# Performance work log

Measured on AMD Instinct MI355X. Metric: run time of the kernel, lower is better.

The kernel has to match this reference:

```python
import jax, jax.numpy as jnp
import numpy as np


def conv1x1(x, w, b):
    # x: [B,C,H,W], w: [O,C], b: [O]
    return jnp.einsum('bchw,oc->bohw', x, w) + b[None, :, None, None]


def conv3x3(x, w, b):
    # x: [B,C,H,W], w: [O,C,3,3]
    y = jax.lax.conv_general_dilated(
        x, w, window_strides=(1, 1), padding='SAME',
        dimension_numbers=('NCHW', 'OIHW', 'NCHW'))
    return y + b[None, :, None, None]


def setup_inputs() -> dict:
    key = jax.random.key(0)
    ks = jax.random.split(key, 20)

    def u(k, shape, fan_in):
        # PyTorch Conv2d default init: uniform(-1/sqrt(fan_in), 1/sqrt(fan_in))
        s = 1.0 / np.sqrt(fan_in)
        return jax.random.uniform(k, shape, jnp.float32, -s, s)

    B, H, W = 4, 64, 64
    return {
        'x':   jax.random.normal(ks[0], (B, 3, H, W), jnp.float32),
        # 1x1 stem convs (weights stored as [O,C])
        'w1':  u(ks[1], (64, 3), 3),        'b1':  u(ks[2], (64,), 3),
        'w2':  u(ks[3], (128, 64), 64),     'b2':  u(ks[4], (128,), 64),
        'w3':  u(ks[5], (256, 128), 128),   'b3':  u(ks[6], (256,), 128),
        # 3x3 conv branch (fan_in = 256*9)
        'wb1': u(ks[7], (256, 256, 3, 3), 256 * 9), 'bb1': u(ks[8], (256,), 256 * 9),
        'wb2': u(ks[9], (256, 256, 3, 3), 256 * 9), 'bb2': u(ks[10], (256,), 256 * 9),
        # q/k/v 1x1 convs
        'wq':  u(ks[11], (256, 256), 256),  'bq':  u(ks[12], (256,), 256),
        'wk':  u(ks[13], (256, 256), 256),  'bk':  u(ks[14], (256,), 256),
        'wv':  u(ks[15], (256, 256), 256),  'bv':  u(ks[16], (256,), 256),
        'alpha': jnp.float32(0.5),
        'beta':  jnp.float32(0.5),
    }


def reference(x, w1, b1, w2, b2, w3, b3, wb1, bb1, wb2, bb2,
              wq, bq, wk, bk, wv, bv, alpha, beta):
    x = jax.nn.relu(conv1x1(x, w1, b1))
    x = jax.nn.relu(conv1x1(x, w2, b2))
    x = jax.nn.relu(conv1x1(x, w3, b3))          # [B,256,H,W]
    conv_out = conv3x3(jax.nn.relu(conv3x3(x, wb1, bb1)), wb2, bb2)
    B, C, H, W = x.shape
    q = conv1x1(x, wq, bq).reshape(B, C, -1)     # [B,C,N]
    k = conv1x1(x, wk, bk).reshape(B, C, -1)     # [B,C,N]
    v = conv1x1(x, wv, bv).reshape(B, C, -1)     # [B,C,N]
    # torch: bmm(k^T, q) -> [B,N,N], softmax over last dim
    attn = jax.nn.softmax(jnp.einsum('bcn,bcm->bnm', k, q), axis=-1)
    # torch: bmm(v, attn) -> [B,C,N]
    attn_out = jnp.einsum('bcn,bnm->bcm', v, attn).reshape(B, C, H, W)
    return alpha * conv_out + beta * attn_out
```

## Files before the change

kernel.cpp:

```cpp
#include <hip/hip_runtime.h>
#include <math.h>

#define NPIX 4096
#define CC   256

typedef __attribute__((ext_vector_type(8))) short bf16x8;
typedef __attribute__((ext_vector_type(4))) float f32x4;

__device__ inline unsigned short f2bf(float f) {
    unsigned u = __builtin_bit_cast(unsigned, f);
    u += 0x7FFF + ((u >> 16) & 1);
    return (unsigned short)(u >> 16);
}
__device__ inline float bf2f(unsigned short h) {
    unsigned u = (unsigned)h << 16;
    return __builtin_bit_cast(float, u);
}
__device__ inline void gl_lds16(const unsigned short* g, unsigned short* l) {
    __builtin_amdgcn_global_load_lds(
        (const __attribute__((address_space(1))) void*)g,
        (__attribute__((address_space(3))) void*)l, 16, 0, 0);
}

__global__ __launch_bounds__(256) void prep_kernel(
    const float* __restrict__ w2, const float* __restrict__ w3,
    const float* __restrict__ wq, const float* __restrict__ wk,
    const float* __restrict__ wv, const float* __restrict__ wb1,
    const float* __restrict__ wb2, const float* __restrict__ bq,
    const float* __restrict__ bk,
    unsigned short* w2b, unsigned short* w3b, unsigned short* wqb,
    unsigned short* wkb, unsigned short* wvb,
    unsigned short* wr1, unsigned short* wr2, float* bqk) {
    int i = blockIdx.x * 256 + threadIdx.x;
    if (i < 8192)  w2b[i] = f2bf(w2[i]);
    if (i < 32768) w3b[i] = f2bf(w3[i]);
    if (i < 65536) { wqb[i] = f2bf(wq[i]); wkb[i] = f2bf(wk[i]); wvb[i] = f2bf(wv[i]); }
    if (i < 256)   { bqk[i] = bq[i]; bqk[256 + i] = bk[i]; }
    if (i < 589824) {
        int o = i / 2304; int r = i - o * 2304; int tap = r >> 8; int c = r & 255;
        wr1[i] = f2bf(wb1[(o * 256 + c) * 9 + tap]);
        wr2[i] = f2bf(wb2[(o * 256 + c) * 9 + tap]);
    }
}

__global__ __launch_bounds__(256) void stem1_kernel(
    const float* __restrict__ x, const float* __restrict__ w1,
    const float* __restrict__ b1, unsigned short* __restrict__ h1T) {
    int idx = blockIdx.x * 256 + threadIdx.x;
    int o = idx & 63;
    int p = (idx >> 6) & 4095;
    int b = idx >> 18;
    const float* xb = x + (size_t)b * 3 * NPIX + p;
    float acc = b1[o];
    acc = fmaf(w1[o * 3 + 0], xb[0],        acc);
    acc = fmaf(w1[o * 3 + 1], xb[NPIX],     acc);
    acc = fmaf(w1[o * 3 + 2], xb[2 * NPIX], acc);
    h1T[idx] = f2bf(fmaxf(acc, 0.f));
}

template<int EPI, int KK>
__global__ __launch_bounds__(256) void gemm_fullk(
    const unsigned short* __restrict__ A, long lda, long sA,
    const unsigned short* __restrict__ BT, long ldb, long sB,
    void* __restrict__ Cp, long ldc, long sC,
    const float* __restrict__ bias, float* __restrict__ aux) {
    constexpr int SPR = KK / 8;
    constexpr int RPI = 64 / SPR;
    __shared__ unsigned short As[128 * KK];
    __shared__ unsigned short Bs[128 * KK];
    const int tid  = threadIdx.x;
    const int lane = tid & 63;
    const int wave = tid >> 6;
    const int wr = (wave >> 1) * 64, wc = (wave & 1) * 64;
    const int l15 = lane & 15, lh = lane >> 4;
    const int sl  = lane & (SPR - 1);
    const int rof = lane / SPR;
    const int z = blockIdx.z;
    const unsigned short* Ab = A  + (size_t)z * sA + (size_t)blockIdx.y * 128 * lda;
    const unsigned short* Bb = BT + (size_t)z * sB + (size_t)blockIdx.x * 128 * ldb;

    f32x4 acc[4][4];
    #pragma unroll
    for (int i = 0; i < 4; ++i)
        #pragma unroll
        for (int j = 0; j < 4; ++j) { f32x4 zr = {0.f, 0.f, 0.f, 0.f}; acc[i][j] = zr; }

    #pragma unroll
    for (int i = 0; i < KK / 16; ++i) {
        int r0  = wave * 32 + i * RPI;
        int row = r0 + rof;
        int cs  = (sl ^ (row & (SPR - 1))) * 8;
        gl_lds16(Ab + (size_t)row * lda + cs, &As[r0 * KK]);
        gl_lds16(Bb + (size_t)row * ldb + cs, &Bs[r0 * KK]);
    }
    __syncthreads();

    #pragma unroll
    for (int ks = 0; ks < KK / 32; ++ks) {
        bf16x8 a[4], b[4];
        #pragma unroll
        for (int f = 0; f < 4; ++f) {
            int ra = wr + f * 16 + l15;
            a[f] = *(const bf16x8*)&As[ra * KK + ((((ks << 2) + lh) ^ (ra & (SPR - 1))) << 3)];
            int rb = wc + f * 16 + l15;
            b[f] = *(const bf16x8*)&Bs[rb * KK + ((((ks << 2) + lh) ^ (rb & (SPR - 1))) << 3)];
        }
        #pragma unroll
        for (int i = 0; i < 4; ++i)
            #pragma unroll
            for (int j = 0; j < 4; ++j)
                acc[i][j] = __builtin_amdgcn_mfma_f32_16x16x32_bf16(
                    a[i], b[j], acc[i][j], 0, 0, 0);
    }

    const int row0 = blockIdx.y * 128 + wr;
    const int col0 = blockIdx.x * 128 + wc;
    unsigned short* OUT = (unsigned short*)Cp + (size_t)z * sC;
    #pragma unroll
    for (int i = 0; i < 4; ++i)
        #pragma unroll
        for (int j = 0; j < 4; ++j) {
            int cgl = col0 + j * 16 + l15;
            float bc = (EPI == 1 || EPI == 2) ? bias[cgl] : 0.f;
            float sc = (EPI == 3) ? aux[(size_t)z * 4096 + cgl] : 1.f;
            #pragma unroll
            for (int q = 0; q < 4; ++q) {
                int r = row0 + i * 16 + lh * 4 + q;
                float v = acc[i][j][q];
                if (EPI == 3) v = (v + bias[r]) * sc;
                else v += bc;
                if (EPI == 1) v = fmaxf(v, 0.f);
                OUT[(size_t)r * ldc + cgl] = f2bf(v);
            }
        }
}

#define PH_ENTER                                            \
    asm volatile("" ::: "memory");                          \
    __builtin_amdgcn_s_barrier();                           \
    asm volatile("s_waitcnt lgkmcnt(0)" ::: "memory");      \
    __builtin_amdgcn_sched_barrier(0);                      \
    __builtin_amdgcn_s_setprio(1);
#define PH_EXIT                                             \
    __builtin_amdgcn_s_setprio(0);                          \
    asm volatile("" ::: "memory");                          \
    __builtin_amdgcn_s_barrier();

#define DO_TILE(CURA, CURB, NXTA, NXTB, KT)                                    \
{                                                                              \
    const int kn_ = (KT) + 1;                                                  \
    bf16x8 aL[4][2], aH[4][2], b01[2][2], b23[2][2];                           \
                                 \
    _Pragma("unroll") for (int f = 0; f < 4; ++f) {                            \
        const unsigned short* rp = &(CURA)[(wr + f * 16 + l15) * 64];          \
        aL[f][0] = *(const bf16x8*)&rp[sa0];                                   \
        aL[f][1] = *(const bf16x8*)&rp[sa1];                                   \
    }                                                                          \
    _Pragma("unroll") for (int f = 0; f < 2; ++f) {                            \
        const unsigned short* rp = &(CURB)[(wc + f * 16 + l15) * 64];          \
        b01[f][0] = *(const bf16x8*)&rp[sa0];                                  \
        b01[f][1] = *(const bf16x8*)&rp[sa1];                                  \
    }                                                                          \
    if (kn_ < T) {                                                             \
        _Pragma("unroll") for (int s = 0; s < 4; ++s) {                        \
            int rb_ = wave * 32 + s * 8;                                       \
            gl_lds16(Ab + (size_t)(rb_ + rof) * lda + (kn_ << 6) + csw,        \
                     &(NXTA)[rb_ * 64]);                                       \
        }                                                                      \
    }                                                                          \
    PH_ENTER;                                                                  \
    _Pragma("unroll") for (int i = 0; i < 4; ++i)                              \
        _Pragma("unroll") for (int j = 0; j < 2; ++j)                          \
            _Pragma("unroll") for (int ks = 0; ks < 2; ++ks)                   \
                acc[i][j] = __builtin_amdgcn_mfma_f32_16x16x32_bf16(           \
                    aL[i][ks], b01[j][ks], acc[i][j], 0, 0, 0);                \
    PH_EXIT;                                                                   \
                                      \
    _Pragma("unroll") for (int f = 0; f < 2; ++f) {                            \
        const unsigned short* rp = &(CURB)[(wc + 32 + f * 16 + l15) * 64];     \
        b23[f][0] = *(const bf16x8*)&rp[sa0];                                  \
        b23[f][1] = *(const bf16x8*)&rp[sa1];                                  \
    }                                                                          \
    if (kn_ < T) {                                                             \
        _Pragma("unroll") for (int s = 0; s < 4; ++s) {                        \
            int rb_ = wave * 32 + s * 8;                                       \
            gl_lds16(Bb + (size_t)(rb_ + rof) * ldb + (kn_ << 6) + csw,        \
                     &(NXTB)[rb_ * 64]);                                       \
        }                                                                      \
    }                                                                          \
    PH_ENTER;                                                                  \
    _Pragma("unroll") for (int i = 0; i < 4; ++i)                              \
        _Pragma("unroll") for (int j = 0; j < 2; ++j)                          \
            _Pragma("unroll") for (int ks = 0; ks < 2; ++ks)                   \
                acc[i][j + 2] = __builtin_amdgcn_mfma_f32_16x16x32_bf16(       \
                    aL[i][ks], b23[j][ks], acc[i][j + 2], 0, 0, 0);            \
    PH_EXIT;                                                                   \
                                                    \
    _Pragma("unroll") for (int f = 0; f < 4; ++f) {                            \
        const unsigned short* rp = &(CURA)[(wr + 64 + f * 16 + l15) * 64];     \
        aH[f][0] = *(const bf16x8*)&rp[sa0];                                   \
        aH[f][1] = *(const bf16x8*)&rp[sa1];                                   \
    }                                                                          \
    PH_ENTER;                                                                  \
    _Pragma("unroll") for (int i = 0; i < 4; ++i)                              \
        _Pragma("unroll") for (int j = 0; j < 2; ++j)                          \
            _Pragma("unroll") for (int ks = 0; ks < 2; ++ks)                   \
                acc[i + 4][j + 2] = __builtin_amdgcn_mfma_f32_16x16x32_bf16(   \
                    aH[i][ks], b23[j][ks], acc[i + 4][j + 2], 0, 0, 0);        \
    PH_EXIT;                                                                   \
                                             \
    asm volatile("s_waitcnt vmcnt(0)" ::: "memory");                           \
    PH_ENTER;                                                                  \
    _Pragma("unroll") for (int i = 0; i < 4; ++i)                              \
        _Pragma("unroll") for (int j = 0; j < 2; ++j)                          \
            _Pragma("unroll") for (int ks = 0; ks < 2; ++ks)                   \
                acc[i + 4][j] = __builtin_amdgcn_mfma_f32_16x16x32_bf16(       \
                    aH[i][ks], b01[j][ks], acc[i + 4][j], 0, 0, 0);            \
    PH_EXIT;                                                                   \
}

template<int EPI>
__global__ __launch_bounds__(512) void gemm256(
    const unsigned short* __restrict__ A, long lda, long sA,
    const unsigned short* __restrict__ BT, long ldb, long sB,
    int Kc, int splits, int nb,
    void* __restrict__ Cp, long ldc, long sC,
    float* __restrict__ aux, float* __restrict__ partial,
    const unsigned short* __restrict__ CV,
    const float* __restrict__ alphaP, const float* __restrict__ betaP,
    int nwgc) {
    __shared__ unsigned short As0[256 * 64], As1[256 * 64];
    __shared__ unsigned short Bs0[256 * 64], Bs1[256 * 64];
    const int orig = blockIdx.x;
    const int wgid = (orig & 7) * nwgc + (orig >> 3);
    int bx, by, sp, z;
    if (EPI == 0) { bx = wgid & 15; by = (wgid >> 4) & 15; z = wgid >> 8; sp = 0; }
    else          { bx = wgid & 15; sp = (wgid >> 4) & (splits - 1); z = wgid / (16 * splits); by = 0; }

    const int tid  = threadIdx.x;
    const int lane = tid & 63;
    const int wave = tid >> 6;
    const int wr = (wave >> 2) * 128;
    const int wc = (wave & 3) * 64;
    const int l15 = lane & 15, lh = lane >> 4;
    const int sl  = lane & 7, rof = lane >> 3;
    const int csw = (sl ^ rof) * 8;
    const int sa0 = ((lh ^ (l15 & 7)) << 3);
    const int sa1 = (((4 + lh) ^ (l15 & 7)) << 3);
    const unsigned short* Ab = A  + (size_t)z * sA + (size_t)by * 256 * lda + (size_t)sp * Kc;
    const unsigned short* Bb = BT + (size_t)z * sB + (size_t)bx * 256 * ldb + (size_t)sp * Kc;

    f32x4 acc[8][4];
    #pragma unroll
    for (int i = 0; i < 8; ++i)
        #pragma unroll
        for (int j = 0; j < 4; ++j) { f32x4 zr = {0.f, 0.f, 0.f, 0.f}; acc[i][j] = zr; }

    const int T = Kc >> 6;
    #pragma unroll
    for (int s = 0; s < 4; ++s) {
        int rb = wave * 32 + s * 8;
        gl_lds16(Ab + (size_t)(rb + rof) * lda + csw, &As0[rb * 64]);
        gl_lds16(Bb + (size_t)(rb + rof) * ldb + csw, &Bs0[rb * 64]);
    }
    asm volatile("s_waitcnt vmcnt(0)" ::: "memory");
    __builtin_amdgcn_s_barrier();

    for (int kt = 0; kt < T; kt += 2) {
        DO_TILE(As0, Bs0, As1, Bs1, kt);
        DO_TILE(As1, Bs1, As0, Bs0, kt + 1);
    }

    if (EPI == 0) {
        unsigned short* OUT = (unsigned short*)Cp + (size_t)z * sC;
        const int row0 = by * 256 + wr;
        const int col0 = bx * 256 + wc;
        float cs4[4] = {0.f, 0.f, 0.f, 0.f};
        #pragma unroll
        for (int i = 0; i < 8; ++i)
            #pragma unroll
            for (int j = 0; j < 4; ++j) {
                int cgl = col0 + j * 16 + l15;
                #pragma unroll
                for (int q = 0; q < 4; ++q) {
                    int r = row0 + i * 16 + lh * 4 + q;
                    unsigned short h = f2bf(__expf(acc[i][j][q]));
                    OUT[(size_t)r * ldc + cgl] = h;
                    cs4[j] += bf2f(h);
                }
            }
        #pragma unroll
        for (int off = 16; off <= 32; off <<= 1)
            #pragma unroll
            for (int j = 0; j < 4; ++j)
                cs4[j] += __shfl_xor(cs4[j], off);
        if (lh == 0) {
            float* part = aux + (((size_t)z * 16 + by) * 2 + (wave >> 2)) * 4096;
            #pragma unroll
            for (int j = 0; j < 4; ++j)
                part[col0 + j * 16 + l15] = cs4[j];
        }
    } else {
        const int col0 = bx * 256 + wc;
        if (splits == 1) {
            float* OUT = (float*)Cp + (size_t)z * sC;
            const unsigned short* CVb = CV + (size_t)z * sC;
            const float al = alphaP[0], be = betaP[0];
            #pragma unroll
            for (int i = 0; i < 8; ++i)
                #pragma unroll
                for (int j = 0; j < 4; ++j) {
                    int cgl = col0 + j * 16 + l15;
                    #pragma unroll
                    for (int q = 0; q < 4; ++q) {
                        int r = wr + i * 16 + lh * 4 + q;
                        size_t o = (size_t)r * ldc + cgl;
                        OUT[o] = al * bf2f(CVb[o]) + be * acc[i][j][q];
                    }
                }
        } else {
            float* P = partial + ((size_t)sp * nb + z) * ((size_t)256 * 4096);
            #pragma unroll
            for (int i = 0; i < 8; ++i)
                #pragma unroll
                for (int j = 0; j < 4; ++j) {
                    int cgl = col0 + j * 16 + l15;
                    #pragma unroll
                    for (int q = 0; q < 4; ++q) {
                        int r = wr + i * 16 + lh * 4 + q;
                        P[(size_t)r * 4096 + cgl] = acc[i][j][q];
                    }
                }
        }
    }
}

__global__ __launch_bounds__(256) void reduce_kernel(
    const float* __restrict__ partial, const unsigned short* __restrict__ cvb,
    const float* __restrict__ alphaP, const float* __restrict__ betaP,
    float* __restrict__ outp, int splits, long chunk) {
    long idx = ((long)blockIdx.x * 256 + threadIdx.x) * 4;
    if (idx >= chunk) return;
    float4 s = *(const float4*)&partial[idx];
    for (int sp = 1; sp < splits; ++sp) {
        float4 p = *(const float4*)&partial[(size_t)sp * chunk + idx];
        s.x += p.x; s.y += p.y; s.z += p.z; s.w += p.w;
    }
    ushort4 c4 = *(const ushort4*)&cvb[idx];
    const float al = alphaP[0], be = betaP[0];
    float4 r;
    r.x = al * bf2f(c4.x) + be * s.x;
    r.y = al * bf2f(c4.y) + be * s.y;
    r.z = al * bf2f(c4.z) + be * s.z;
    r.w = al * bf2f(c4.w) + be * s.w;
    *(float4*)&outp[idx] = r;
}

__global__ __launch_bounds__(256) void recip_kernel(
    const float* __restrict__ part, float* __restrict__ rcp) {
    int idx = blockIdx.x * 256 + threadIdx.x;
    int z = idx >> 12, n = idx & 4095;
    const float* pb = part + (size_t)z * 32 * 4096 + n;
    float s = 0.f;
    #pragma unroll 8
    for (int t = 0; t < 32; ++t) s += pb[(size_t)t * 4096];
    rcp[idx] = 1.f / s;
}

template<int PIXOUT>
__global__ __launch_bounds__(256) void conv3_v2(
    const unsigned short* __restrict__ X, const unsigned short* __restrict__ Wr,
    const float* __restrict__ bias, void* __restrict__ Outp) {
    __shared__ unsigned short wt[9 * 128 * 40];
    __shared__ unsigned short patch[264 * 40];
    const int tid  = threadIdx.x;
    const int lane = tid & 63;
    const int wave = tid >> 6;
    const int l15 = lane & 15, lh = lane >> 4;
    const int oh = blockIdx.x & 1;
    const int b  = blockIdx.x >> 1;
    const int h0 = blockIdx.y;
    const int wy = (wave >> 1) * 64, wx = (wave & 1) * 64;
    const int obase = PIXOUT ? wx : wy;
    const int pbase = PIXOUT ? wy : wx;
    const unsigned short* Xb  = X + (size_t)b * (NPIX * CC);
    const unsigned short* Wro = Wr + (size_t)oh * 128 * 2304;

    f32x4 acc[4][4];
    #pragma unroll
    for (int i = 0; i < 4; ++i)
        #pragma unroll
        for (int j = 0; j < 4; ++j) { f32x4 zr = {0.f, 0.f, 0.f, 0.f}; acc[i][j] = zr; }

    for (int c0 = 0; c0 < 256; c0 += 32) {
        __syncthreads();
        #pragma unroll
        for (int t = 0; t < 5; ++t) {
            int q = t * 256 + tid;
            if (q < 1056) {
                int slot = q >> 2, cg = (q & 3) * 8;
                int r = slot / 66, w = slot - r * 66;
                int hh = h0 * 2 - 1 + r, ww = w - 1;
                int4 v = make_int4(0, 0, 0, 0);
                if ((unsigned)hh < 64u && (unsigned)ww < 64u)
                    v = *(const int4*)&Xb[(size_t)(hh * 64 + ww) * 256 + c0 + cg];
                *(int4*)&patch[slot * 40 + cg] = v;
            }
        }
        #pragma unroll
        for (int t = 0; t < 18; ++t) {
            int q = t * 256 + tid;
            int o = q / 36, rem = q - o * 36;
            int tap = rem >> 2, cg = (rem & 3) * 8;
            int4 v = *(const int4*)&Wro[(size_t)o * 2304 + tap * 256 + c0 + cg];
            *(int4*)&wt[(tap * 128 + o) * 40 + cg] = v;
        }
        __syncthreads();
        #pragma unroll
        for (int tap = 0; tap < 9; ++tap) {
            const int dy = tap / 3 - 1, dx = tap % 3 - 1;
            bf16x8 wf[4], pf[4];
            #pragma unroll
            for (int f = 0; f < 4; ++f) {
                int o = obase + f * 16 + l15;
                wf[f] = *(const bf16x8*)&wt[(tap * 128 + o) * 40 + lh * 8];
                int p = pbase + f * 16 + l15;
                int slot = ((p >> 6) + dy + 1) * 66 + (p & 63) + dx + 1;
                pf[f] = *(const bf16x8*)&patch[slot * 40 + lh * 8];
            }
            #pragma unroll
            for (int i = 0; i < 4; ++i)
                #pragma unroll
                for (int j = 0; j < 4; ++j) {
                    if (PIXOUT)
                        acc[i][j] = __builtin_amdgcn_mfma_f32_16x16x32_bf16(
                            pf[i], wf[j], acc[i][j], 0, 0, 0);
                    else
                        acc[i][j] = __builtin_amdgcn_mfma_f32_16x16x32_bf16(
                            wf[i], pf[j], acc[i][j], 0, 0, 0);
                }
        }
    }

    const int P0 = h0 * 128;
    if (PIXOUT) {
        unsigned short* O = (unsigned short*)Outp + (size_t)b * (NPIX * CC);
        #pragma unroll
        for (int i = 0; i < 4; ++i)
            #pragma unroll
            for (int j = 0; j < 4; ++j) {
                int o = oh * 128 + obase + j * 16 + l15;
                float bb = bias[o];
                #pragma unroll
                for (int q = 0; q < 4; ++q) {
                    int p = pbase + i * 16 + lh * 4 + q;
                    float v = fmaxf(acc[i][j][q] + bb, 0.f);
                    O[(size_t)(P0 + p) * CC + o] = f2bf(v);
                }
            }
    } else {
        unsigned short* O = (unsigned short*)Outp + (size_t)b * (CC * NPIX);
        #pragma unroll
        for (int i = 0; i < 4; ++i)
            #pragma unroll
            for (int j = 0; j < 4; ++j) {
                #pragma unroll
                for (int q = 0; q < 4; ++q) {
                    int o = oh * 128 + obase + i * 16 + lh * 4 + q;
                    int p = pbase + j * 16 + l15;
                    O[(size_t)o * NPIX + P0 + p] = f2bf(acc[i][j][q] + bias[o]);
                }
            }
    }
}

extern "C" void kernel_launch(void* const* d_in, const int* in_sizes, int n_in,
                              void* d_out, int out_size, void* d_ws, size_t ws_size,
                              hipStream_t stream) {
    const float* x   = (const float*)d_in[0];
    const float* w1  = (const float*)d_in[1];  const float* b1  = (const float*)d_in[2];
    const float* w2  = (const float*)d_in[3];  const float* b2  = (const float*)d_in[4];
    const float* w3  = (const float*)d_in[5];  const float* b3  = (const float*)d_in[6];
    const float* wb1 = (const float*)d_in[7];  const float* bb1 = (const float*)d_in[8];
    const float* wb2 = (const float*)d_in[9];  const float* bb2 = (const float*)d_in[10];
    const float* wq  = (const float*)d_in[11]; const float* bq  = (const float*)d_in[12];
    const float* wk  = (const float*)d_in[13]; const float* bk  = (const float*)d_in[14];
    const float* wv  = (const float*)d_in[15]; const float* bv  = (const float*)d_in[16];
    const float* alpha = (const float*)d_in[17];
    const float* beta  = (const float*)d_in[18];

    const size_t MB = 1 << 20;
    char* wsb = (char*)d_ws;
    unsigned short* x3T = (unsigned short*)(wsb + 0 * MB);
    unsigned short* qkT = (unsigned short*)(wsb + 8 * MB);
    unsigned short* cv  = (unsigned short*)(wsb + 24 * MB);
    unsigned short* t1T = (unsigned short*)(wsb + 32 * MB);
    unsigned short* h1T = (unsigned short*)(wsb + 32 * MB);
    unsigned short* h2T = (unsigned short*)(wsb + 34 * MB);
    unsigned short* vB  = (unsigned short*)(wsb + 40 * MB);
    unsigned short* w2b = (unsigned short*)(wsb + 48 * MB);
    unsigned short* w3b = w2b + 8192;
    unsigned short* wqb = w3b + 32768;
    unsigned short* wkb = wqb + 65536;
    unsigned short* wvb = wkb + 65536;
    unsigned short* wr1 = wvb + 65536;
    unsigned short* wr2 = wr1 + 589824;
    float*          bqk  = (float*)(wsb + 51 * MB);
    float*          part = (float*)(wsb + 52 * MB);
    float*          rcp  = (float*)(wsb + 54 * MB);
    unsigned short* ST   = (unsigned short*)(wsb + 55 * MB);
    float* out = (float*)d_out;
    const long ONEM = (long)CC * NPIX;
    const long SS = 4096L * 4096;

    int nb, splits;
    if      (ws_size >= (size_t)247 * MB) { nb = 4; splits = 4;  }
    else if (ws_size >= (size_t)183 * MB) { nb = 2; splits = 8;  }
    else if (ws_size >= (size_t)151 * MB) { nb = 1; splits = 16; }
    else if (ws_size >= (size_t)119 * MB) { nb = 1; splits = 8;  }
    else if (ws_size >= (size_t)103 * MB) { nb = 1; splits = 4;  }
    else                                  { nb = 1; splits = 1;  }
    float* pvpart = (float*)(wsb + (size_t)(55 + nb * 32) * MB);

    prep_kernel<<<2304, 256, 0, stream>>>(w2, w3, wq, wk, wv, wb1, wb2, bq, bk,
                                          w2b, w3b, wqb, wkb, wvb, wr1, wr2, bqk);
    stem1_kernel<<<4096, 256, 0, stream>>>(x, w1, b1, h1T);

    gemm_fullk<1, 64><<<dim3(1, 32, 4), 256, 0, stream>>>(
        h1T, 64, 4096L * 64, w2b, 64, 0,
        h2T, 128, 4096L * 128, b2, nullptr);
    gemm_fullk<1, 128><<<dim3(2, 32, 4), 256, 0, stream>>>(
        h2T, 128, 4096L * 128, w3b, 128, 0,
        x3T, 256, 4096L * 256, b3, nullptr);
    gemm_fullk<2, 256><<<dim3(4, 32, 4), 256, 0, stream>>>(
        x3T, 256, 4096L * 256, wqb, 256, 0,
        qkT, 512, 4096L * 512, bqk, nullptr);
    conv3_v2<1><<<dim3(8, 32), 256, 0, stream>>>(x3T, wr1, bb1, t1T);
    conv3_v2<0><<<dim3(8, 32), 256, 0, stream>>>(t1T, wr2, bb2, cv);

    for (int b0 = 0; b0 < 4; b0 += nb) {
        int nwgS = 256 * nb;
        gemm256<0><<<nwgS, 512, 0, stream>>>(
            qkT + (size_t)b0 * 4096 * 512, 512, 4096L * 512,
            qkT + (size_t)b0 * 4096 * 512 + 256, 512, 4096L * 512,
            256, 1, nb, ST, 4096, SS,
            part, nullptr, nullptr, nullptr, nullptr, nwgS / 8);
        recip_kernel<<<nb * 16, 256, 0, stream>>>(part, rcp);
        gemm_fullk<3, 256><<<dim3(32, 2, nb), 256, 0, stream>>>(
            wvb, 256, 0,
            x3T + (size_t)b0 * 4096 * 256, 256, 4096L * 256,
            vB, 4096, 256L * 4096, bv, rcp);
        int nwgP = 16 * splits * nb;
        gemm256<4><<<nwgP, 512, 0, stream>>>(
            vB, 4096, 256L * 4096, ST, 4096, SS,
            4096 / splits, splits, nb,
            out + (size_t)b0 * ONEM, 4096, ONEM,
            nullptr, pvpart, cv + (size_t)b0 * ONEM, alpha, beta, nwgP / 8);
        if (splits > 1)
            reduce_kernel<<<nb * 1024, 256, 0, stream>>>(
                pvpart, cv + (size_t)b0 * ONEM, alpha, beta,
                out + (size_t)b0 * ONEM, splits, (long)nb * ONEM);
    }
}
```

Baseline: 245.4 us.

## Store attention scores and scaled V in FP8 and run PV GEMM with FP8 MFMA

The exp(S) matrix and the normalized V are now written as FP8 (with scale factors of 1/16 and 256 to keep values in range) instead of bf16. A new FP8 PV GEMM kernel then uses 16x16x32 fp8 MFMA, which halves the bytes of the dominant 4096x4096 score matrix traffic. Split-K partials are stored as bf16 instead of fp32, and the split/batch configuration changes to nb=4, splits=8. This trades numerical accuracy, since FP8 softmax weights and bf16 partials are lossy, for lower memory traffic and higher MFMA throughput.

```diff
diff --git a/kernel.cpp b/kernel.cpp
--- a/kernel.cpp
+++ b/kernel.cpp
@@ -16,7 +16,11 @@
     unsigned u = (unsigned)h << 16;
     return __builtin_bit_cast(float, u);
 }
-__device__ inline void gl_lds16(const unsigned short* g, unsigned short* l) {
+__device__ inline unsigned char f2fp8(float f) {
+    int p = __builtin_amdgcn_cvt_pk_fp8_f32(f, f, 0, false);
+    return (unsigned char)(p & 0xff);
+}
+__device__ inline void gl_lds16(const void* g, void* l) {
     __builtin_amdgcn_global_load_lds(
         (const __attribute__((address_space(1))) void*)g,
         (__attribute__((address_space(3))) void*)l, 16, 0, 0);
@@ -115,24 +119,37 @@
 
     const int row0 = blockIdx.y * 128 + wr;
     const int col0 = blockIdx.x * 128 + wc;
-    unsigned short* OUT = (unsigned short*)Cp + (size_t)z * sC;
-    #pragma unroll
-    for (int i = 0; i < 4; ++i)
-        #pragma unroll
-        for (int j = 0; j < 4; ++j) {
-            int cgl = col0 + j * 16 + l15;
-            float bc = (EPI == 1 || EPI == 2) ? bias[cgl] : 0.f;
-            float sc = (EPI == 3) ? aux[(size_t)z * 4096 + cgl] : 1.f;
-            #pragma unroll
-            for (int q = 0; q < 4; ++q) {
-                int r = row0 + i * 16 + lh * 4 + q;
-                float v = acc[i][j][q];
-                if (EPI == 3) v = (v + bias[r]) * sc;
-                else v += bc;
-                if (EPI == 1) v = fmaxf(v, 0.f);
-                OUT[(size_t)r * ldc + cgl] = f2bf(v);
-            }
-        }
+    if (EPI == 3) {
+        unsigned char* O8 = (unsigned char*)Cp + (size_t)z * sC;
+        #pragma unroll
+        for (int i = 0; i < 4; ++i)
+            #pragma unroll
+            for (int j = 0; j < 4; ++j) {
+                int cgl = col0 + j * 16 + l15;
+                float sc = aux[(size_t)z * 4096 + cgl];
+                #pragma unroll
+                for (int q = 0; q < 4; ++q) {
+                    int r = row0 + i * 16 + lh * 4 + q;
+                    O8[(size_t)r * ldc + cgl] = f2fp8((acc[i][j][q] + bias[r]) * sc);
+                }
+            }
+    } else {
+        unsigned short* OUT = (unsigned short*)Cp + (size_t)z * sC;
+        #pragma unroll
+        for (int i = 0; i < 4; ++i)
+            #pragma unroll
+            for (int j = 0; j < 4; ++j) {
+                int cgl = col0 + j * 16 + l15;
+                float bc = bias[cgl];
+                #pragma unroll
+                for (int q = 0; q < 4; ++q) {
+                    int r = row0 + i * 16 + lh * 4 + q;
+                    float v = acc[i][j][q] + bc;
+                    if (EPI == 1) v = fmaxf(v, 0.f);
+                    OUT[(size_t)r * ldc + cgl] = f2bf(v);
+                }
+            }
+    }
 }
 
 #define PH_ENTER                                            \
@@ -150,7 +167,6 @@
 {                                                                              \
     const int kn_ = (KT) + 1;                                                  \
     bf16x8 aL[4][2], aH[4][2], b01[2][2], b23[2][2];                           \
-                                 \
     _Pragma("unroll") for (int f = 0; f < 4; ++f) {                            \
         const unsigned short* rp = &(CURA)[(wr + f * 16 + l15) * 64];          \
         aL[f][0] = *(const bf16x8*)&rp[sa0];                                   \
@@ -175,7 +191,6 @@
                 acc[i][j] = __builtin_amdgcn_mfma_f32_16x16x32_bf16(           \
                     aL[i][ks], b01[j][ks], acc[i][j], 0, 0, 0);                \
     PH_EXIT;                                                                   \
-                                      \
     _Pragma("unroll") for (int f = 0; f < 2; ++f) {                            \
         const unsigned short* rp = &(CURB)[(wc + 32 + f * 16 + l15) * 64];     \
         b23[f][0] = *(const bf16x8*)&rp[sa0];                                  \
@@ -195,7 +210,6 @@
                 acc[i][j + 2] = __builtin_amdgcn_mfma_f32_16x16x32_bf16(       \
                     aL[i][ks], b23[j][ks], acc[i][j + 2], 0, 0, 0);            \
     PH_EXIT;                                                                   \
-                                                    \
     _Pragma("unroll") for (int f = 0; f < 4; ++f) {                            \
         const unsigned short* rp = &(CURA)[(wr + 64 + f * 16 + l15) * 64];     \
         aH[f][0] = *(const bf16x8*)&rp[sa0];                                   \
@@ -208,7 +222,6 @@
                 acc[i + 4][j + 2] = __builtin_amdgcn_mfma_f32_16x16x32_bf16(   \
                     aH[i][ks], b23[j][ks], acc[i + 4][j + 2], 0, 0, 0);        \
     PH_EXIT;                                                                   \
-                                             \
     asm volatile("s_waitcnt vmcnt(0)" ::: "memory");                           \
     PH_ENTER;                                                                  \
     _Pragma("unroll") for (int i = 0; i < 4; ++i)                              \
@@ -219,23 +232,16 @@
     PH_EXIT;                                                                   \
 }
 
-template<int EPI>
-__global__ __launch_bounds__(512) void gemm256(
+__global__ __launch_bounds__(512) void gemm_s(
     const unsigned short* __restrict__ A, long lda, long sA,
     const unsigned short* __restrict__ BT, long ldb, long sB,
-    int Kc, int splits, int nb,
-    void* __restrict__ Cp, long ldc, long sC,
-    float* __restrict__ aux, float* __restrict__ partial,
-    const unsigned short* __restrict__ CV,
-    const float* __restrict__ alphaP, const float* __restrict__ betaP,
-    int nwgc) {
+    unsigned char* __restrict__ Cp, long ldc, long sC,
+    float* __restrict__ aux, int nwgc) {
     __shared__ unsigned short As0[256 * 64], As1[256 * 64];
     __shared__ unsigned short Bs0[256 * 64], Bs1[256 * 64];
     const int orig = blockIdx.x;
     const int wgid = (orig & 7) * nwgc + (orig >> 3);
-    int bx, by, sp, z;
-    if (EPI == 0) { bx = wgid & 15; by = (wgid >> 4) & 15; z = wgid >> 8; sp = 0; }
-    else          { bx = wgid & 15; sp = (wgid >> 4) & (splits - 1); z = wgid / (16 * splits); by = 0; }
+    const int bx = wgid & 15, by = (wgid >> 4) & 15, z = wgid >> 8;
 
     const int tid  = threadIdx.x;
     const int lane = tid & 63;
@@ -247,8 +253,8 @@
     const int csw = (sl ^ rof) * 8;
     const int sa0 = ((lh ^ (l15 & 7)) << 3);
     const int sa1 = (((4 + lh) ^ (l15 & 7)) << 3);
-    const unsigned short* Ab = A  + (size_t)z * sA + (size_t)by * 256 * lda + (size_t)sp * Kc;
-    const unsigned short* Bb = BT + (size_t)z * sB + (size_t)bx * 256 * ldb + (size_t)sp * Kc;
+    const unsigned short* Ab = A  + (size_t)z * sA + (size_t)by * 256 * lda;
+    const unsigned short* Bb = BT + (size_t)z * sB + (size_t)bx * 256 * ldb;
 
     f32x4 acc[8][4];
     #pragma unroll
@@ -256,7 +262,7 @@
         #pragma unroll
         for (int j = 0; j < 4; ++j) { f32x4 zr = {0.f, 0.f, 0.f, 0.f}; acc[i][j] = zr; }
 
-    const int T = Kc >> 6;
+    const int T = 4;
     #pragma unroll
     for (int s = 0; s < 4; ++s) {
         int rb = wave * 32 + s * 8;
@@ -271,11 +277,124 @@
         DO_TILE(As1, Bs1, As0, Bs0, kt + 1);
     }
 
-    if (EPI == 0) {
-        unsigned short* OUT = (unsigned short*)Cp + (size_t)z * sC;
-        const int row0 = by * 256 + wr;
-        const int col0 = bx * 256 + wc;
-        float cs4[4] = {0.f, 0.f, 0.f, 0.f};
+    unsigned char* OUT = Cp + (size_t)z * sC;
+    const int row0 = by * 256 + wr;
+    const int col0 = bx * 256 + wc;
+    float cs4[4] = {0.f, 0.f, 0.f, 0.f};
+    #pragma unroll
+    for (int i = 0; i < 8; ++i)
+        #pragma unroll
+        for (int j = 0; j < 4; ++j) {
+            int cgl = col0 + j * 16 + l15;
+            #pragma unroll
+            for (int q = 0; q < 4; ++q) {
+                int r = row0 + i * 16 + lh * 4 + q;
+                float e = __expf(acc[i][j][q]) * 0.0625f;
+                OUT[(size_t)r * ldc + cgl] = f2fp8(e);
+                cs4[j] += e;
+            }
+        }
+    #pragma unroll
+    for (int off = 16; off <= 32; off <<= 1)
+        #pragma unroll
+        for (int j = 0; j < 4; ++j)
+            cs4[j] += __shfl_xor(cs4[j], off);
+    if (lh == 0) {
+        float* part = aux + (((size_t)z * 16 + by) * 2 + (wave >> 2)) * 4096;
+        #pragma unroll
+        for (int j = 0; j < 4; ++j)
+            part[col0 + j * 16 + l15] = cs4[j];
+    }
+}
+
+__global__ __launch_bounds__(512) void gemm_pv8(
+    const unsigned char* __restrict__ A, long lda, long sA,
+    const unsigned char* __restrict__ BT, long ldb, long sB,
+    int Kc, int splits, int nb,
+    float* __restrict__ outp, long ldc, long sC,
+    unsigned short* __restrict__ partial,
+    const unsigned short* __restrict__ CV,
+    const float* __restrict__ alphaP, const float* __restrict__ betaP,
+    int nwgc) {
+    __shared__ unsigned char As[2][256 * 64];
+    __shared__ unsigned char Bs[2][256 * 64];
+    const int orig = blockIdx.x;
+    const int wgid = (orig & 7) * nwgc + (orig >> 3);
+    const int bx = wgid & 15;
+    const int sp = (wgid >> 4) % splits;
+    const int z  = wgid / (16 * splits);
+    const int tid  = threadIdx.x;
+    const int lane = tid & 63;
+    const int wave = tid >> 6;
+    const int wr = (wave >> 2) * 128;
+    const int wc = (wave & 3) * 64;
+    const int l15 = lane & 15, lh = lane >> 4;
+    const int srow = lane >> 2, sslot = lane & 3;
+    const unsigned char* Ab = A  + (size_t)z * sA + (size_t)sp * Kc;
+    const unsigned char* Bb = BT + (size_t)z * sB + (size_t)bx * 256 * ldb + (size_t)sp * Kc;
+
+    f32x4 acc[8][4];
+    #pragma unroll
+    for (int i = 0; i < 8; ++i)
+        #pragma unroll
+        for (int j = 0; j < 4; ++j) { f32x4 zr = {0.f, 0.f, 0.f, 0.f}; acc[i][j] = zr; }
+
+    auto STAGE = [&](int buf, int k0) {
+        #pragma unroll
+        for (int s = 0; s < 2; ++s) {
+            int rb  = wave * 32 + s * 16;
+            int row = rb + srow;
+            int cs  = (sslot ^ (row & 3)) << 4;
+            gl_lds16(Ab + (size_t)row * lda + k0 + cs, &As[buf][rb * 64]);
+            gl_lds16(Bb + (size_t)row * ldb + k0 + cs, &Bs[buf][rb * 64]);
+        }
+    };
+
+    STAGE(0, 0);
+    const int T = Kc >> 6;
+    for (int t = 0; t < T; ++t) {
+        const int cur = t & 1;
+        if (t + 1 < T) {
+            STAGE(cur ^ 1, (t + 1) << 6);
+            asm volatile("s_waitcnt vmcnt(4)" ::: "memory");
+        } else {
+            asm volatile("s_waitcnt vmcnt(0)" ::: "memory");
+        }
+        __builtin_amdgcn_s_barrier();
+        asm volatile("" ::: "memory");
+        __builtin_amdgcn_s_setprio(1);
+        #pragma unroll
+        for (int ks = 0; ks < 2; ++ks) {
+            long a[8], b[4];
+            #pragma unroll
+            for (int f = 0; f < 8; ++f) {
+                int row = wr + f * 16 + l15;
+                int ad  = row * 64 + ((((ks << 1) + (lh >> 1)) ^ (row & 3)) << 4) + ((lh & 1) << 3);
+                a[f] = *(const long*)&As[cur][ad];
+            }
+            #pragma unroll
+            for (int f = 0; f < 4; ++f) {
+                int row = wc + f * 16 + l15;
+                int ad  = row * 64 + ((((ks << 1) + (lh >> 1)) ^ (row & 3)) << 4) + ((lh & 1) << 3);
+                b[f] = *(const long*)&Bs[cur][ad];
+            }
+            #pragma unroll
+            for (int i = 0; i < 8; ++i)
+                #pragma unroll
+                for (int j = 0; j < 4; ++j)
+                    acc[i][j] = __builtin_amdgcn_mfma_f32_16x16x32_fp8_fp8(
+                        a[i], b[j], acc[i][j], 0, 0, 0);
+        }
+        __builtin_amdgcn_s_setprio(0);
+        asm volatile("" ::: "memory");
+        __builtin_amdgcn_s_barrier();
+    }
+
+    const int col0 = bx * 256 + wc;
+    if (splits == 1) {
+        float* OUT = outp + (size_t)z * sC;
+        const unsigned short* CVb = CV + (size_t)z * sC;
+        const float al = alphaP[0], be = betaP[0] * (1.f / 256.f);
         #pragma unroll
         for (int i = 0; i < 8; ++i)
             #pragma unroll
@@ -283,76 +402,45 @@
                 int cgl = col0 + j * 16 + l15;
                 #pragma unroll
                 for (int q = 0; q < 4; ++q) {
-                    int r = row0 + i * 16 + lh * 4 + q;
-                    unsigned short h = f2bf(__expf(acc[i][j][q]));
-                    OUT[(size_t)r * ldc + cgl] = h;
-                    cs4[j] += bf2f(h);
+                    int r = wr + i * 16 + lh * 4 + q;
+                    size_t o = (size_t)r * ldc + cgl;
+                    OUT[o] = al * bf2f(CVb[o]) + be * acc[i][j][q];
                 }
             }
-        #pragma unroll
-        for (int off = 16; off <= 32; off <<= 1)
-            #pragma unroll
-            for (int j = 0; j < 4; ++j)
-                cs4[j] += __shfl_xor(cs4[j], off);
-        if (lh == 0) {
-            float* part = aux + (((size_t)z * 16 + by) * 2 + (wave >> 2)) * 4096;
-            #pragma unroll
-            for (int j = 0; j < 4; ++j)
-                part[col0 + j * 16 + l15] = cs4[j];
-        }
     } else {
-        const int col0 = bx * 256 + wc;
-        if (splits == 1) {
-            float* OUT = (float*)Cp + (size_t)z * sC;
-            const unsigned short* CVb = CV + (size_t)z * sC;
-            const float al = alphaP[0], be = betaP[0];
-            #pragma unroll
-            for (int i = 0; i < 8; ++i)
-                #pragma unroll
-                for (int j = 0; j < 4; ++j) {
-                    int cgl = col0 + j * 16 + l15;
-                    #pragma unroll
-                    for (int q = 0; q < 4; ++q) {
-                        int r = wr + i * 16 + lh * 4 + q;
-                        size_t o = (size_t)r * ldc + cgl;
-                        OUT[o] = al * bf2f(CVb[o]) + be * acc[i][j][q];
-                    }
+        unsigned short* P = partial + ((size_t)sp * nb + z) * ((size_t)256 * 4096);
+        #pragma unroll
+        for (int i = 0; i < 8; ++i)
+            #pragma unroll
+            for (int j = 0; j < 4; ++j) {
+                int cgl = col0 + j * 16 + l15;
+                #pragma unroll
+                for (int q = 0; q < 4; ++q) {
+                    int r = wr + i * 16 + lh * 4 + q;
+                    P[(size_t)r * 4096 + cgl] = f2bf(acc[i][j][q]);
                 }
-        } else {
-            float* P = partial + ((size_t)sp * nb + z) * ((size_t)256 * 4096);
-            #pragma unroll
-            for (int i = 0; i < 8; ++i)
-                #pragma unroll
-                for (int j = 0; j < 4; ++j) {
-                    int cgl = col0 + j * 16 + l15;
-                    #pragma unroll
-                    for (int q = 0; q < 4; ++q) {
-                        int r = wr + i * 16 + lh * 4 + q;
-                        P[(size_t)r * 4096 + cgl] = acc[i][j][q];
-                    }
-                }
-        }
+            }
     }
 }
 
 __global__ __launch_bounds__(256) void reduce_kernel(
-    const float* __restrict__ partial, const unsigned short* __restrict__ cvb,
+    const unsigned short* __restrict__ partial, const unsigned short* __restrict__ cvb,
     const float* __restrict__ alphaP, const float* __restrict__ betaP,
     float* __restrict__ outp, int splits, long chunk) {
     long idx = ((long)blockIdx.x * 256 + threadIdx.x) * 4;
     if (idx >= chunk) return;
-    float4 s = *(const float4*)&partial[idx];
-    for (int sp = 1; sp < splits; ++sp) {
-        float4 p = *(const float4*)&partial[(size_t)sp * chunk + idx];
-        s.x += p.x; s.y += p.y; s.z += p.z; s.w += p.w;
+    float s0 = 0.f, s1 = 0.f, s2 = 0.f, s3 = 0.f;
+    for (int sp = 0; sp < splits; ++sp) {
+        ushort4 p = *(const ushort4*)&partial[(size_t)sp * chunk + idx];
+        s0 += bf2f(p.x); s1 += bf2f(p.y); s2 += bf2f(p.z); s3 += bf2f(p.w);
     }
     ushort4 c4 = *(const ushort4*)&cvb[idx];
-    const float al = alphaP[0], be = betaP[0];
+    const float al = alphaP[0], be = betaP[0] * (1.f / 256.f);
     float4 r;
-    r.x = al * bf2f(c4.x) + be * s.x;
-    r.y = al * bf2f(c4.y) + be * s.y;
-    r.z = al * bf2f(c4.z) + be * s.z;
-    r.w = al * bf2f(c4.w) + be * s.w;
+    r.x = al * bf2f(c4.x) + be * s0;
+    r.y = al * bf2f(c4.y) + be * s1;
+    r.z = al * bf2f(c4.z) + be * s2;
+    r.w = al * bf2f(c4.w) + be * s3;
     *(float4*)&outp[idx] = r;
 }
 
@@ -364,7 +452,7 @@
     float s = 0.f;
     #pragma unroll 8
     for (int t = 0; t < 32; ++t) s += pb[(size_t)t * 4096];
-    rcp[idx] = 1.f / s;
+    rcp[idx] = 256.f / s;
 }
 
 template<int PIXOUT>
@@ -497,7 +585,7 @@
     unsigned short* t1T = (unsigned short*)(wsb + 32 * MB);
     unsigned short* h1T = (unsigned short*)(wsb + 32 * MB);
     unsigned short* h2T = (unsigned short*)(wsb + 34 * MB);
-    unsigned short* vB  = (unsigned short*)(wsb + 40 * MB);
+    unsigned char*  vB8 = (unsigned char*)(wsb + 40 * MB);
     unsigned short* w2b = (unsigned short*)(wsb + 48 * MB);
     unsigned short* w3b = w2b + 8192;
     unsigned short* wqb = w3b + 32768;
@@ -508,19 +596,17 @@
     float*          bqk  = (float*)(wsb + 51 * MB);
     float*          part = (float*)(wsb + 52 * MB);
     float*          rcp  = (float*)(wsb + 54 * MB);
-    unsigned short* ST   = (unsigned short*)(wsb + 55 * MB);
+    unsigned char*  ST8  = (unsigned char*)(wsb + 55 * MB);
     float* out = (float*)d_out;
     const long ONEM = (long)CC * NPIX;
     const long SS = 4096L * 4096;
 
     int nb, splits;
-    if      (ws_size >= (size_t)247 * MB) { nb = 4; splits = 4;  }
-    else if (ws_size >= (size_t)183 * MB) { nb = 2; splits = 8;  }
-    else if (ws_size >= (size_t)151 * MB) { nb = 1; splits = 16; }
-    else if (ws_size >= (size_t)119 * MB) { nb = 1; splits = 8;  }
-    else if (ws_size >= (size_t)103 * MB) { nb = 1; splits = 4;  }
-    else                                  { nb = 1; splits = 1;  }
-    float* pvpart = (float*)(wsb + (size_t)(55 + nb * 32) * MB);
+    if      (ws_size >= (size_t)183 * MB) { nb = 4; splits = 8; }
+    else if (ws_size >= (size_t)119 * MB) { nb = 2; splits = 8; }
+    else if (ws_size >= (size_t)87  * MB) { nb = 1; splits = 8; }
+    else                                  { nb = 1; splits = 1; }
+    unsigned short* pvpart = (unsigned short*)(wsb + (size_t)(55 + nb * 16) * MB);
 
     prep_kernel<<<2304, 256, 0, stream>>>(w2, w3, wq, wk, wv, wb1, wb2, bq, bk,
                                           w2b, w3b, wqb, wkb, wvb, wr1, wr2, bqk);
@@ -540,22 +626,21 @@
 
     for (int b0 = 0; b0 < 4; b0 += nb) {
         int nwgS = 256 * nb;
-        gemm256<0><<<nwgS, 512, 0, stream>>>(
+        gemm_s<<<nwgS, 512, 0, stream>>>(
             qkT + (size_t)b0 * 4096 * 512, 512, 4096L * 512,
             qkT + (size_t)b0 * 4096 * 512 + 256, 512, 4096L * 512,
-            256, 1, nb, ST, 4096, SS,
-            part, nullptr, nullptr, nullptr, nullptr, nwgS / 8);
+            ST8, 4096, SS, part, nwgS / 8);
         recip_kernel<<<nb * 16, 256, 0, stream>>>(part, rcp);
         gemm_fullk<3, 256><<<dim3(32, 2, nb), 256, 0, stream>>>(
             wvb, 256, 0,
             x3T + (size_t)b0 * 4096 * 256, 256, 4096L * 256,
-            vB, 4096, 256L * 4096, bv, rcp);
+            vB8, 4096, 256L * 4096, bv, rcp);
         int nwgP = 16 * splits * nb;
-        gemm256<4><<<nwgP, 512, 0, stream>>>(
-            vB, 4096, 256L * 4096, ST, 4096, SS,
+        gemm_pv8<<<nwgP, 512, 0, stream>>>(
+            vB8, 4096, 256L * 4096, ST8, 4096, SS,
             4096 / splits, splits, nb,
             out + (size_t)b0 * ONEM, 4096, ONEM,
-            nullptr, pvpart, cv + (size_t)b0 * ONEM, alpha, beta, nwgP / 8);
+            pvpart, cv + (size_t)b0 * ONEM, alpha, beta, nwgP / 8);
         if (splits > 1)
             reduce_kernel<<<nb * 1024, 256, 0, stream>>>(
                 pvpart, cv + (size_t)b0 * ONEM, alpha, beta,
```

Measured after the change: 253.1 us. +3.1%, slower.

## Deepen B-operand prefetch in split-K GEMM, store bf16 partials, raise split count

Applied to the files above, without the earlier changes.

The GEMM main loop now stages B two tiles ahead and A one tile ahead, each split into halves issued between MFMA phases. The trailing vmcnt(0) becomes vmcnt(4), so global-to-LDS loads stay in flight across the tile boundary. Split-K partial sums are now written and read as bf16 instead of fp32, which halves partial-buffer traffic and allows doubling the split count for the same workspace. The bf16 partials lose accuracy in the attention output sum, and the split index now uses modulo, which permits non-power-of-two split counts.

```diff
diff --git a/kernel.cpp b/kernel.cpp
--- a/kernel.cpp
+++ b/kernel.cpp
@@ -16,7 +16,7 @@
     unsigned u = (unsigned)h << 16;
     return __builtin_bit_cast(float, u);
 }
-__device__ inline void gl_lds16(const unsigned short* g, unsigned short* l) {
+__device__ inline void gl_lds16(const void* g, void* l) {
     __builtin_amdgcn_global_load_lds(
         (const __attribute__((address_space(1))) void*)g,
         (__attribute__((address_space(3))) void*)l, 16, 0, 0);
@@ -146,11 +146,11 @@
     asm volatile("" ::: "memory");                          \
     __builtin_amdgcn_s_barrier();
 
-#define DO_TILE(CURA, CURB, NXTA, NXTB, KT)                                    \
+#define DO_TILE(CURA, CURB, NXTA, KT)                                          \
 {                                                                              \
-    const int kn_ = (KT) + 1;                                                  \
+    const int kn1 = (KT) + 1, kn2 = (KT) + 2;                                  \
     bf16x8 aL[4][2], aH[4][2], b01[2][2], b23[2][2];                           \
-                                 \
+                                       \
     _Pragma("unroll") for (int f = 0; f < 4; ++f) {                            \
         const unsigned short* rp = &(CURA)[(wr + f * 16 + l15) * 64];          \
         aL[f][0] = *(const bf16x8*)&rp[sa0];                                   \
@@ -161,13 +161,7 @@
         b01[f][0] = *(const bf16x8*)&rp[sa0];                                  \
         b01[f][1] = *(const bf16x8*)&rp[sa1];                                  \
     }                                                                          \
-    if (kn_ < T) {                                                             \
-        _Pragma("unroll") for (int s = 0; s < 4; ++s) {                        \
-            int rb_ = wave * 32 + s * 8;                                       \
-            gl_lds16(Ab + (size_t)(rb_ + rof) * lda + (kn_ << 6) + csw,        \
-                     &(NXTA)[rb_ * 64]);                                       \
-        }                                                                      \
-    }                                                                          \
+    if (kn1 < T) STAGE_A(NXTA, kn1 << 6, 0);                                   \
     PH_ENTER;                                                                  \
     _Pragma("unroll") for (int i = 0; i < 4; ++i)                              \
         _Pragma("unroll") for (int j = 0; j < 2; ++j)                          \
@@ -175,19 +169,13 @@
                 acc[i][j] = __builtin_amdgcn_mfma_f32_16x16x32_bf16(           \
                     aL[i][ks], b01[j][ks], acc[i][j], 0, 0, 0);                \
     PH_EXIT;                                                                   \
-                                      \
+                                            \
     _Pragma("unroll") for (int f = 0; f < 2; ++f) {                            \
         const unsigned short* rp = &(CURB)[(wc + 32 + f * 16 + l15) * 64];     \
         b23[f][0] = *(const bf16x8*)&rp[sa0];                                  \
         b23[f][1] = *(const bf16x8*)&rp[sa1];                                  \
     }                                                                          \
-    if (kn_ < T) {                                                             \
-        _Pragma("unroll") for (int s = 0; s < 4; ++s) {                        \
-            int rb_ = wave * 32 + s * 8;                                       \
-            gl_lds16(Bb + (size_t)(rb_ + rof) * ldb + (kn_ << 6) + csw,        \
-                     &(NXTB)[rb_ * 64]);                                       \
-        }                                                                      \
-    }                                                                          \
+    if (kn1 < T) STAGE_A(NXTA, kn1 << 6, 1);                                   \
     PH_ENTER;                                                                  \
     _Pragma("unroll") for (int i = 0; i < 4; ++i)                              \
         _Pragma("unroll") for (int j = 0; j < 2; ++j)                          \
@@ -195,12 +183,13 @@
                 acc[i][j + 2] = __builtin_amdgcn_mfma_f32_16x16x32_bf16(       \
                     aL[i][ks], b23[j][ks], acc[i][j + 2], 0, 0, 0);            \
     PH_EXIT;                                                                   \
-                                                    \
+           \
     _Pragma("unroll") for (int f = 0; f < 4; ++f) {                            \
         const unsigned short* rp = &(CURA)[(wr + 64 + f * 16 + l15) * 64];     \
         aH[f][0] = *(const bf16x8*)&rp[sa0];                                   \
         aH[f][1] = *(const bf16x8*)&rp[sa1];                                   \
     }                                                                          \
+    if (kn2 < T) STAGE_B(CURB, kn2 << 6, 0);                                   \
     PH_ENTER;                                                                  \
     _Pragma("unroll") for (int i = 0; i < 4; ++i)                              \
         _Pragma("unroll") for (int j = 0; j < 2; ++j)                          \
@@ -208,15 +197,19 @@
                 acc[i + 4][j + 2] = __builtin_amdgcn_mfma_f32_16x16x32_bf16(   \
                     aH[i][ks], b23[j][ks], acc[i + 4][j + 2], 0, 0, 0);        \
     PH_EXIT;                                                                   \
-                                             \
-    asm volatile("s_waitcnt vmcnt(0)" ::: "memory");                           \
+            \
+    if (kn2 < T) STAGE_B(CURB, kn2 << 6, 1);                                   \
     PH_ENTER;                                                                  \
     _Pragma("unroll") for (int i = 0; i < 4; ++i)                              \
         _Pragma("unroll") for (int j = 0; j < 2; ++j)                          \
             _Pragma("unroll") for (int ks = 0; ks < 2; ++ks)                   \
                 acc[i + 4][j] = __builtin_amdgcn_mfma_f32_16x16x32_bf16(       \
                     aH[i][ks], b01[j][ks], acc[i + 4][j], 0, 0, 0);            \
-    PH_EXIT;                                                                   \
+    __builtin_amdgcn_s_setprio(0);                                             \
+    if (kn2 < T) { asm volatile("s_waitcnt vmcnt(4)" ::: "memory"); }          \
+    else         { asm volatile("s_waitcnt vmcnt(0)" ::: "memory"); }          \
+    asm volatile("" ::: "memory");                                             \
+    __builtin_amdgcn_s_barrier();                                              \
 }
 
 template<int EPI>
@@ -225,7 +218,7 @@
     const unsigned short* __restrict__ BT, long ldb, long sB,
     int Kc, int splits, int nb,
     void* __restrict__ Cp, long ldc, long sC,
-    float* __restrict__ aux, float* __restrict__ partial,
+    float* __restrict__ aux, unsigned short* __restrict__ partial,
     const unsigned short* __restrict__ CV,
     const float* __restrict__ alphaP, const float* __restrict__ betaP,
     int nwgc) {
@@ -235,7 +228,7 @@
     const int wgid = (orig & 7) * nwgc + (orig >> 3);
     int bx, by, sp, z;
     if (EPI == 0) { bx = wgid & 15; by = (wgid >> 4) & 15; z = wgid >> 8; sp = 0; }
-    else          { bx = wgid & 15; sp = (wgid >> 4) & (splits - 1); z = wgid / (16 * splits); by = 0; }
+    else          { bx = wgid & 15; sp = (wgid >> 4) % splits; z = wgid / (16 * splits); by = 0; }
 
     const int tid  = threadIdx.x;
     const int lane = tid & 63;
@@ -244,7 +237,6 @@
     const int wc = (wave & 3) * 64;
     const int l15 = lane & 15, lh = lane >> 4;
     const int sl  = lane & 7, rof = lane >> 3;
-    const int csw = (sl ^ rof) * 8;
     const int sa0 = ((lh ^ (l15 & 7)) << 3);
     const int sa1 = (((4 + lh) ^ (l15 & 7)) << 3);
     const unsigned short* Ab = A  + (size_t)z * sA + (size_t)by * 256 * lda + (size_t)sp * Kc;
@@ -256,19 +248,35 @@
         #pragma unroll
         for (int j = 0; j < 4; ++j) { f32x4 zr = {0.f, 0.f, 0.f, 0.f}; acc[i][j] = zr; }
 
+    auto STAGE_A = [&](unsigned short* dst, int k0, int h) {
+        #pragma unroll
+        for (int s = 0; s < 2; ++s) {
+            int rb  = h * 128 + s * 64 + wave * 8;
+            int row = rb + rof;
+            int cs  = (sl ^ (row & 7)) * 8;
+            gl_lds16(Ab + (size_t)row * lda + k0 + cs, &dst[rb * 64]);
+        }
+    };
+    auto STAGE_B = [&](unsigned short* dst, int k0, int h) {
+        #pragma unroll
+        for (int s = 0; s < 2; ++s) {
+            int rb  = h * 128 + s * 64 + wave * 8;
+            int row = rb + rof;
+            int cs  = (sl ^ (row & 7)) * 8;
+            gl_lds16(Bb + (size_t)row * ldb + k0 + cs, &dst[rb * 64]);
+        }
+    };
+
     const int T = Kc >> 6;
-    #pragma unroll
-    for (int s = 0; s < 4; ++s) {
-        int rb = wave * 32 + s * 8;
-        gl_lds16(Ab + (size_t)(rb + rof) * lda + csw, &As0[rb * 64]);
-        gl_lds16(Bb + (size_t)(rb + rof) * ldb + csw, &Bs0[rb * 64]);
-    }
-    asm volatile("s_waitcnt vmcnt(0)" ::: "memory");
+    STAGE_A(As0, 0, 0); STAGE_A(As0, 0, 1);
+    STAGE_B(Bs0, 0, 0); STAGE_B(Bs0, 0, 1);
+    STAGE_B(Bs1, 64, 0); STAGE_B(Bs1, 64, 1);
+    asm volatile("s_waitcnt vmcnt(4)" ::: "memory");
     __builtin_amdgcn_s_barrier();
 
     for (int kt = 0; kt < T; kt += 2) {
-        DO_TILE(As0, Bs0, As1, Bs1, kt);
-        DO_TILE(As1, Bs1, As0, Bs0, kt + 1);
+        DO_TILE(As0, Bs0, As1, kt);
+        DO_TILE(As1, Bs1, As0, kt + 1);
     }
 
     if (EPI == 0) {
@@ -319,7 +327,7 @@
                     }
                 }
         } else {
-            float* P = partial + ((size_t)sp * nb + z) * ((size_t)256 * 4096);
+            unsigned short* P = partial + ((size_t)sp * nb + z) * ((size_t)256 * 4096);
             #pragma unroll
             for (int i = 0; i < 8; ++i)
                 #pragma unroll
@@ -328,7 +336,7 @@
                     #pragma unroll
                     for (int q = 0; q < 4; ++q) {
                         int r = wr + i * 16 + lh * 4 + q;
-                        P[(size_t)r * 4096 + cgl] = acc[i][j][q];
+                        P[(size_t)r * 4096 + cgl] = f2bf(acc[i][j][q]);
                     }
                 }
         }
@@ -336,23 +344,23 @@
 }
 
 __global__ __launch_bounds__(256) void reduce_kernel(
-    const float* __restrict__ partial, const unsigned short* __restrict__ cvb,
+    const unsigned short* __restrict__ partial, const unsigned short* __restrict__ cvb,
     const float* __restrict__ alphaP, const float* __restrict__ betaP,
     float* __restrict__ outp, int splits, long chunk) {
     long idx = ((long)blockIdx.x * 256 + threadIdx.x) * 4;
     if (idx >= chunk) return;
-    float4 s = *(const float4*)&partial[idx];
-    for (int sp = 1; sp < splits; ++sp) {
-        float4 p = *(const float4*)&partial[(size_t)sp * chunk + idx];
-        s.x += p.x; s.y += p.y; s.z += p.z; s.w += p.w;
+    float s0 = 0.f, s1 = 0.f, s2 = 0.f, s3 = 0.f;
+    for (int sp = 0; sp < splits; ++sp) {
+        ushort4 p = *(const ushort4*)&partial[(size_t)sp * chunk + idx];
+        s0 += bf2f(p.x); s1 += bf2f(p.y); s2 += bf2f(p.z); s3 += bf2f(p.w);
     }
     ushort4 c4 = *(const ushort4*)&cvb[idx];
     const float al = alphaP[0], be = betaP[0];
     float4 r;
-    r.x = al * bf2f(c4.x) + be * s.x;
-    r.y = al * bf2f(c4.y) + be * s.y;
-    r.z = al * bf2f(c4.z) + be * s.z;
-    r.w = al * bf2f(c4.w) + be * s.w;
+    r.x = al * bf2f(c4.x) + be * s0;
+    r.y = al * bf2f(c4.y) + be * s1;
+    r.z = al * bf2f(c4.z) + be * s2;
+    r.w = al * bf2f(c4.w) + be * s3;
     *(float4*)&outp[idx] = r;
 }
 
@@ -514,13 +522,11 @@
     const long SS = 4096L * 4096;
 
     int nb, splits;
-    if      (ws_size >= (size_t)247 * MB) { nb = 4; splits = 4;  }
-    else if (ws_size >= (size_t)183 * MB) { nb = 2; splits = 8;  }
-    else if (ws_size >= (size_t)151 * MB) { nb = 1; splits = 16; }
-    else if (ws_size >= (size_t)119 * MB) { nb = 1; splits = 8;  }
-    else if (ws_size >= (size_t)103 * MB) { nb = 1; splits = 4;  }
+    if      (ws_size >= (size_t)247 * MB) { nb = 4; splits = 8;  }
+    else if (ws_size >= (size_t)183 * MB) { nb = 2; splits = 16; }
+    else if (ws_size >= (size_t)119 * MB) { nb = 1; splits = 16; }
     else                                  { nb = 1; splits = 1;  }
-    float* pvpart = (float*)(wsb + (size_t)(55 + nb * 32) * MB);
+    unsigned short* pvpart = (unsigned short*)(wsb + (size_t)(55 + nb * 32) * MB);
 
     prep_kernel<<<2304, 256, 0, stream>>>(w2, w3, wq, wk, wv, wb1, wb2, bq, bk,
                                           w2b, w3b, wqb, wkb, wvb, wr1, wr2, bqk);
```

Result: slower. 254.3 us (+3.6%).
